# Kernel optimization log

Hardware: AMD Instinct MI355X
Metric: run time of the kernel (lower is better)

Reference implementation:

```python
import jax, jax.numpy as jnp
import numpy as np

B, NPG = 64, 512          # graphs, nodes per graph
N_TOTAL = B * NPG
LIG = 128                 # ligand nodes per graph (segment 0); rest are protein (segment 1)
BOX = 40.0                # Angstrom box for random coords -> realistic radius-graph density
INTER_CUTOFF = 10.0       # normalize_coord is identity (scale=1)
INTRA_CUTOFF = 8.0


def setup_inputs() -> dict:
    key = jax.random.key(0)
    X = jax.random.uniform(key, (N_TOTAL, 1, 3), dtype=jnp.float32) * BOX
    batch_id = jnp.repeat(jnp.arange(B, dtype=jnp.int32), NPG)
    local = jnp.tile(jnp.arange(NPG, dtype=jnp.int32), B)
    segment_id = (local >= LIG).astype(jnp.int32)
    is_global = jnp.logical_or(local == 0, local == LIG)  # one global node per segment
    return {"X": X, "batch_id": batch_id, "segment_id": segment_id, "is_global": is_global}


def _radial_edges(X, src_dst, cutoff):
    # src_dst: [E, 2] node indices; X: [N, C, 3], channel 0 holds coords
    p = X[:, 0][src_dst]                              # [E, 2, 3]
    dist = jnp.linalg.norm(p[:, 0] - p[:, 1], axis=-1)
    return src_dst[dist <= cutoff].T                  # [2, E']


def reference(X, batch_id, segment_id, is_global):
    N = batch_id.shape[0]
    nB = int(batch_id[-1]) + 1
    lengths = jax.ops.segment_sum(jnp.ones_like(batch_id), batch_id, num_segments=nB)
    max_n = int(jnp.max(lengths))
    offsets = jnp.concatenate([jnp.zeros((1,), lengths.dtype), jnp.cumsum(lengths)[:-1]])
    gni = jnp.arange(N)
    gni2lni = gni - offsets[batch_id]                 # local node index within its graph

    # Dense [N, max_n] same-batch mask via cumsum trick (O(N*max_n))
    same_bid = jnp.zeros((N, max_n), jnp.float32)
    same_bid = same_bid.at[gni, lengths[batch_id] - 1].set(1.0)
    same_bid = 1.0 - jnp.cumsum(same_bid, axis=-1)
    same_bid = jnp.concatenate([jnp.ones((N, 1), jnp.float32), same_bid[:, :-1]], axis=-1)
    same_bid = same_bid.at[gni, gni2lni].set(0.0)     # remove self edges

    row, col = jnp.nonzero(same_bid)                  # all same-graph candidate pairs
    col = col + offsets[batch_id[row]]                # local col -> global node index

    row_global = is_global[row]
    col_global = is_global[col]
    not_global = jnp.logical_not(jnp.logical_or(row_global, col_global))
    row_seg = segment_id[row]
    col_seg = segment_id[col]

    # intra-protein context edges (segment 1, within 8A)
    sel = (row_seg == col_seg) & (row_seg == 1) & not_global
    ctx_edges = _radial_edges(X, jnp.stack([row[sel], col[sel]], axis=1), INTRA_CUTOFF)

    # inter ligand-protein edges (within 10A)
    sel = (row_seg != col_seg) & not_global
    ir, ic = row[sel], col[sel]
    inter_edges = _radial_edges(X, jnp.stack([ir, ic], axis=1), INTER_CUTOFF)
    if inter_edges.shape[1] == 0:
        inter_edges = jnp.array([[ir[0], ic[0]], [ic[0], ir[0]]], dtype=inter_edges.dtype)

    reduced_inter_edge_batchid = batch_id[inter_edges[0][inter_edges[0] < inter_edges[1]]]
    reduced_inter_edge_offsets = offsets[reduced_inter_edge_batchid]

    # global<->same-segment edges and global<->global edges appended to context
    sel = (row_seg == col_seg) & jnp.logical_not(not_global)
    global_normal = jnp.stack([row[sel], col[sel]])
    sel = row_global & col_global
    global_global = jnp.stack([row[sel], col[sel]])
    ctx_edges = jnp.concatenate([ctx_edges, global_normal, global_global], axis=1)

    return ctx_edges, inter_edges, reduced_inter_edge_batchid, reduced_inter_edge_offsets
```

## Files before the change

### kernel.cpp

```cpp
#include <hip/hip_runtime.h>

#define NB 64
#define NPG 512
#define LIG 128
#define NBLK 1024
#define RPB 32
#define THREADS 512

__device__ __forceinline__ float dist2(float dx, float dy, float dz) {
    return __fadd_rn(__fadd_rn(__fmul_rn(dx, dx), __fmul_rn(dy, dy)), __fmul_rn(dz, dz));
}
#define T10 __uint_as_float(0x42C80001u)
#define T8  __uint_as_float(0x42800001u)

__global__ __launch_bounds__(THREADS) void count_kernel(const float* __restrict__ X,
                                                        unsigned long long* __restrict__ gmask,
                                                        int* __restrict__ bp) {
    __shared__ float s[NPG * 3];
    __shared__ unsigned long long smask[RPB * 8];
    __shared__ int rc[RPB], ri[RPB];
    const int b = blockIdx.x;
    const int g = b >> 4;
    const int h = b & 15;
    const int t = threadIdx.x;
    const int lane = t & 63;
    const int w = t >> 6;
    if (t < 384) ((float4*)s)[t] = ((const float4*)X)[g * 384 + t];
    if (t < RPB * 8) smask[t] = 0ull;
    __syncthreads();

    float cx[8], cy[8], cz[8];
#pragma unroll
    for (int k = 0; k < 8; ++k) {
        const int c = k * 64 + lane;
        cx[k] = s[3 * c]; cy[k] = s[3 * c + 1]; cz[k] = s[3 * c + 2];
    }

#pragma unroll
    for (int j = 0; j < 4; ++j) {
        const int lr = w * 4 + j;
        const int r = h * 32 + lr;
        const float px = s[3 * r], py = s[3 * r + 1], pz = s[3 * r + 2];
        int cc = 0, ci = 0;
        if (h < 4) {
            if (r != 0) {
                unsigned long long mm[6];
#pragma unroll
                for (int k = 2; k < 8; ++k) {
                    unsigned long long m =
                        __ballot(dist2(px - cx[k], py - cy[k], pz - cz[k]) <= T10);
                    if (k == 2) m &= ~1ull;
                    mm[k - 2] = m;
                    ci += __popcll(m);
                }
                if (lane == 0) {
#pragma unroll
                    for (int k = 0; k < 6; ++k) smask[lr * 8 + 2 + k] = mm[k];
                }
            }
        } else if (r != LIG) {
            unsigned long long mm[8];
#pragma unroll
            for (int k = 0; k < 2; ++k) {
                unsigned long long m =
                    __ballot(dist2(px - cx[k], py - cy[k], pz - cz[k]) <= T10);
                if (k == 0) m &= ~1ull;
                mm[k] = m;
                ci += __popcll(m);
            }
            const int kr = r >> 6;
            const unsigned long long selfbit = 1ull << (r & 63);
#pragma unroll
            for (int k = 2; k < 8; ++k) {
                unsigned long long m =
                    __ballot(dist2(px - cx[k], py - cy[k], pz - cz[k]) <= T8);
                if (k == 2) m &= ~1ull;
                if (k == kr) m &= ~selfbit;
                mm[k] = m;
                cc += __popcll(m);
            }
            if (lane == 0) {
#pragma unroll
                for (int k = 0; k < 8; ++k) smask[lr * 8 + k] = mm[k];
            }
        }
        if (lane == 0) { rc[lr] = cc; ri[lr] = ci; }
    }
    __syncthreads();
    if (t < RPB * 8) gmask[(size_t)b * (RPB * 8) + t] = smask[t];
    if (t < 64) {
        int c = (t < RPB) ? rc[t] : 0;
        int i = (t < RPB) ? ri[t] : 0;
#pragma unroll
        for (int off = 32; off >= 1; off >>= 1) {
            c += __shfl_down(c, off, 64);
            i += __shfl_down(i, off, 64);
        }
        if (t == 0) {
            bp[b] = c;
            bp[NBLK + b] = i;
            bp[2 * NBLK + b] = (h < 4) ? i : 0;
        }
    }
}

__global__ __launch_bounds__(THREADS) void emit_kernel(const unsigned long long* __restrict__ gmask,
                                                       const int* __restrict__ bp,
                                                       int* __restrict__ out) {
    __shared__ unsigned long long smask[RPB * 8];
    __shared__ int sc[RPB], si[RPB];
    __shared__ int blkb[3], tot[3], sint;
    const int b = blockIdx.x;
    const int g = b >> 4;
    const int h = b & 15;
    const int t = threadIdx.x;
    const int lane = t & 63;
    const int w = t >> 6;
    const unsigned long long lmask = (1ull << lane) - 1ull;
    const int gn = g * NPG;

    if (t < RPB * 8) smask[t] = gmask[(size_t)b * (RPB * 8) + t];

    if (w < 3) {
        const int base = w * NBLK + lane * 16;
        int v[16]; int sum = 0;
#pragma unroll
        for (int i = 0; i < 16; ++i) { v[i] = bp[base + i]; sum += v[i]; }
        int incl = sum;
#pragma unroll
        for (int off = 1; off < 64; off <<= 1) {
            int n = __shfl_up(incl, off, 64);
            if (lane >= off) incl += n;
        }
        if (lane == (b >> 4)) {
            int e = incl - sum;
            const int idx = b & 15;
            for (int i = 0; i < idx; ++i) e += v[i];
            blkb[w] = e;
        }
        if (lane == 63) tot[w] = incl;
    }
    __syncthreads();

    if (t < RPB) {
        int mc = 0, mi = 0;
        if (h < 4) {
#pragma unroll
            for (int k = 2; k < 8; ++k) mi += __popcll(smask[t * 8 + k]);
        } else {
            mi = __popcll(smask[t * 8 + 0]) + __popcll(smask[t * 8 + 1]);
#pragma unroll
            for (int k = 2; k < 8; ++k) mc += __popcll(smask[t * 8 + k]);
        }
        int ic = mc, ii = mi;
#pragma unroll
        for (int off = 1; off < 32; off <<= 1) {
            int a0 = __shfl_up(ic, off, 64);
            int a1 = __shfl_up(ii, off, 64);
            if (lane >= off) { ic += a0; ii += a1; }
        }
        sc[t] = blkb[0] + ic - mc;
        si[t] = blkb[1] + ii - mi;
        if (t == RPB - 1) sint = ii;
    }
    __syncthreads();

    const int Eci = tot[0];
    const int Ei  = tot[1];
    const int Er  = tot[2];
    const int Ectx = Eci + NB * 1020 + NB * 2;

    int* ctx_src   = out;
    int* ctx_dst   = out + Ectx;
    int* inter_src = out + 2 * Ectx;
    int* inter_dst = inter_src + Ei;
    int* red_bid   = out + 2 * Ectx + 2 * Ei;
    int* red_off   = red_bid + Er;

    for (int j = 0; j < 4; ++j) {
        const int lr = w * 4 + j;
        const int r = h * 32 + lr;
        const int row = gn + r;

        unsigned long long m[8];
#pragma unroll
        for (int k = 0; k < 8; ++k) m[k] = smask[lr * 8 + k];

        if (h < 4) {
            if (r == 0) {
                for (int k = 0; k < 2; ++k) {
                    const int c = k * 64 + lane;
                    if (c >= 1 && c < LIG) {
                        const int pos = Eci + g * 1020 + (c - 1);
                        ctx_src[pos] = row; ctx_dst[pos] = gn + c;
                    }
                }
                if (lane == 0) {
                    const int pos = Eci + NB * 1020 + g * 2;
                    ctx_src[pos] = row; ctx_dst[pos] = gn + LIG;
                }
            } else {
                int ib = si[lr];
#pragma unroll
                for (int k = 2; k < 8; ++k) {
                    if (m[k]) {
                        if ((m[k] >> lane) & 1ull) {
                            const int c = k * 64 + lane;
                            const int p = __popcll(m[k] & lmask);
                            inter_src[ib + p] = row; inter_dst[ib + p] = gn + c;
                        }
                        ib += __popcll(m[k]);
                    }
                }
                if (lane == 0) {
                    const int pos = Eci + g * 1020 + (LIG - 1) + (r - 1);
                    ctx_src[pos] = row; ctx_dst[pos] = gn;
                }
            }
        } else {
            if (r == LIG) {
                for (int k = 2; k < 8; ++k) {
                    const int c = k * 64 + lane;
                    if (c > LIG) {
                        const int pos = Eci + g * 1020 + 2 * (LIG - 1) + (c - LIG - 1);
                        ctx_src[pos] = row; ctx_dst[pos] = gn + c;
                    }
                }
                if (lane == 0) {
                    const int pos = Eci + NB * 1020 + g * 2 + 1;
                    ctx_src[pos] = row; ctx_dst[pos] = gn;
                }
            } else {
                int ib = si[lr];
#pragma unroll
                for (int k = 0; k < 2; ++k) {
                    if (m[k]) {
                        if ((m[k] >> lane) & 1ull) {
                            const int c = k * 64 + lane;
                            const int pos = ib + __popcll(m[k] & lmask);
                            inter_src[pos] = row; inter_dst[pos] = gn + c;
                        }
                        ib += __popcll(m[k]);
                    }
                }
                int cb = sc[lr];
#pragma unroll
                for (int k = 2; k < 8; ++k) {
                    if (m[k]) {
                        if ((m[k] >> lane) & 1ull) {
                            const int c = k * 64 + lane;
                            const int pos = cb + __popcll(m[k] & lmask);
                            ctx_src[pos] = row; ctx_dst[pos] = gn + c;
                        }
                        cb += __popcll(m[k]);
                    }
                }
                if (lane == 0) {
                    const int pos = Eci + g * 1020 + 2 * (LIG - 1) + (NPG - LIG - 1) + (r - LIG - 1);
                    ctx_src[pos] = row; ctx_dst[pos] = gn + LIG;
                }
            }
        }
    }

    if (h < 4) {
        const int rb0 = blkb[2];
        const int n = sint;
        for (int i = t; i < n; i += THREADS) {
            red_bid[rb0 + i] = g;
            red_off[rb0 + i] = gn;
        }
    }
}

extern "C" void kernel_launch(void* const* d_in, const int* in_sizes, int n_in,
                              void* d_out, int out_size, void* d_ws, size_t ws_size,
                              hipStream_t stream) {
    (void)in_sizes; (void)n_in; (void)out_size; (void)ws_size;
    const float* X = (const float*)d_in[0];
    int* ws = (int*)d_ws;
    int* bp = ws;
    unsigned long long* gmask =
        (unsigned long long*)(ws + 4096);
    int* out = (int*)d_out;

    count_kernel<<<NBLK, THREADS, 0, stream>>>(X, gmask, bp);
    emit_kernel<<<NBLK, THREADS, 0, stream>>>(gmask, bp, out);
}
```

Baseline: 79.84 us.

## Fuse count and emit kernels via in-kernel spin-waited global prefix scan

Merges the count and emit passes into one kernel. Each block publishes its packed (ctx, inter) counts with a flag bit to a workspace array, then spin-waits on all 1024 entries to compute its exclusive offsets, so the mask never round-trips through global memory and one launch is saved. Adds a memset launch, and correctness depends on all 1024 blocks being co-resident. That is attempted via launch_bounds(512,8), but a guard-limited spin could otherwise deadlock or produce wrong offsets. Counts are packed into 21-bit fields of a 64-bit word.

```diff
diff --git a/kernel.cpp b/kernel.cpp
--- a/kernel.cpp
+++ b/kernel.cpp
@@ -13,18 +13,32 @@
 #define T10 __uint_as_float(0x42C80001u)
 #define T8  __uint_as_float(0x42800001u)
 
-__global__ __launch_bounds__(THREADS) void count_kernel(const float* __restrict__ X,
-                                                        unsigned long long* __restrict__ gmask,
-                                                        int* __restrict__ bp) {
+#define F21 0x1FFFFFull
+
+__device__ __forceinline__ unsigned long long pk_triple(unsigned long long v, int j) {
+    unsigned long long ci = v & F21;
+    unsigned long long cc = (v >> 21) & F21;
+    unsigned long long red = (j < 4) ? ci : 0ull;
+    return (cc << 42) | (ci << 21) | red;
+}
+
+__global__ __launch_bounds__(THREADS, 8) void fused_kernel(const float* __restrict__ X,
+                                                           unsigned long long* __restrict__ pk,
+                                                           int* __restrict__ out) {
     __shared__ float s[NPG * 3];
     __shared__ unsigned long long smask[RPB * 8];
     __shared__ int rc[RPB], ri[RPB];
+    __shared__ int sc[RPB], si[RPB];
+    __shared__ unsigned long long sblkb, stot;
+    __shared__ int sint;
+
     const int b = blockIdx.x;
     const int g = b >> 4;
     const int h = b & 15;
     const int t = threadIdx.x;
     const int lane = t & 63;
     const int w = t >> 6;
+
     if (t < 384) ((float4*)s)[t] = ((const float4*)X)[g * 384 + t];
     if (t < RPB * 8) smask[t] = 0ull;
     __syncthreads();
@@ -87,71 +101,63 @@
         if (lane == 0) { rc[lr] = cc; ri[lr] = ci; }
     }
     __syncthreads();
-    if (t < RPB * 8) gmask[(size_t)b * (RPB * 8) + t] = smask[t];
-    if (t < 64) {
-        int c = (t < RPB) ? rc[t] : 0;
-        int i = (t < RPB) ? ri[t] : 0;
+
+    if (w == 0) {
+        int c = (lane < RPB) ? rc[lane] : 0;
+        int ii = (lane < RPB) ? ri[lane] : 0;
 #pragma unroll
         for (int off = 32; off >= 1; off >>= 1) {
             c += __shfl_down(c, off, 64);
-            i += __shfl_down(i, off, 64);
-        }
-        if (t == 0) {
-            bp[b] = c;
-            bp[NBLK + b] = i;
-            bp[2 * NBLK + b] = (h < 4) ? i : 0;
-        }
-    }
-}
-
-__global__ __launch_bounds__(THREADS) void emit_kernel(const unsigned long long* __restrict__ gmask,
-                                                       const int* __restrict__ bp,
-                                                       int* __restrict__ out) {
-    __shared__ unsigned long long smask[RPB * 8];
-    __shared__ int sc[RPB], si[RPB];
-    __shared__ int blkb[3], tot[3], sint;
-    const int b = blockIdx.x;
-    const int g = b >> 4;
-    const int h = b & 15;
-    const int t = threadIdx.x;
-    const int lane = t & 63;
-    const int w = t >> 6;
-    const unsigned long long lmask = (1ull << lane) - 1ull;
-    const int gn = g * NPG;
-
-    if (t < RPB * 8) smask[t] = gmask[(size_t)b * (RPB * 8) + t];
-
-    if (w < 3) {
-        const int base = w * NBLK + lane * 16;
-        int v[16]; int sum = 0;
-#pragma unroll
-        for (int i = 0; i < 16; ++i) { v[i] = bp[base + i]; sum += v[i]; }
-        int incl = sum;
+            ii += __shfl_down(ii, off, 64);
+        }
+        if (lane == 0) {
+            const unsigned long long q = (1ull << 63) |
+                ((unsigned long long)(unsigned)c << 21) | (unsigned long long)(unsigned)ii;
+            __hip_atomic_store(&pk[b], q, __ATOMIC_RELAXED, __HIP_MEMORY_SCOPE_AGENT);
+        }
+        const int base = lane * 16;
+        unsigned long long sum = 0;
+#pragma unroll
+        for (int j = 0; j < 16; ++j) {
+            unsigned long long v =
+                __hip_atomic_load(&pk[base + j], __ATOMIC_RELAXED, __HIP_MEMORY_SCOPE_AGENT);
+            int guard = 0;
+            while (!(v >> 63) && ++guard < (1 << 20)) {
+                __builtin_amdgcn_s_sleep(8);
+                v = __hip_atomic_load(&pk[base + j], __ATOMIC_RELAXED, __HIP_MEMORY_SCOPE_AGENT);
+            }
+            sum += pk_triple(v, j);
+        }
+        unsigned long long incl = sum;
 #pragma unroll
         for (int off = 1; off < 64; off <<= 1) {
-            int n = __shfl_up(incl, off, 64);
+            unsigned long long n = __shfl_up(incl, off, 64);
             if (lane >= off) incl += n;
         }
         if (lane == (b >> 4)) {
-            int e = incl - sum;
+            unsigned long long e = incl - sum;
             const int idx = b & 15;
-            for (int i = 0; i < idx; ++i) e += v[i];
-            blkb[w] = e;
-        }
-        if (lane == 63) tot[w] = incl;
-    }
-    __syncthreads();
+            for (int jj = 0; jj < idx; ++jj) {
+                unsigned long long v =
+                    __hip_atomic_load(&pk[base + jj], __ATOMIC_RELAXED, __HIP_MEMORY_SCOPE_AGENT);
+                e += pk_triple(v, jj);
+            }
+            sblkb = e;
+        }
+        if (lane == 63) stot = incl;
+    }
+    __syncthreads();
+
+    const int blkb0 = (int)((sblkb >> 42) & F21);
+    const int blkb1 = (int)((sblkb >> 21) & F21);
+    const int blkb2 = (int)(sblkb & F21);
+    const int Eci = (int)((stot >> 42) & F21);
+    const int Ei  = (int)((stot >> 21) & F21);
+    const int Er  = (int)(stot & F21);
 
     if (t < RPB) {
-        int mc = 0, mi = 0;
-        if (h < 4) {
-#pragma unroll
-            for (int k = 2; k < 8; ++k) mi += __popcll(smask[t * 8 + k]);
-        } else {
-            mi = __popcll(smask[t * 8 + 0]) + __popcll(smask[t * 8 + 1]);
-#pragma unroll
-            for (int k = 2; k < 8; ++k) mc += __popcll(smask[t * 8 + k]);
-        }
+        const int mc = rc[t];
+        const int mi = ri[t];
         int ic = mc, ii = mi;
 #pragma unroll
         for (int off = 1; off < 32; off <<= 1) {
@@ -159,15 +165,14 @@
             int a1 = __shfl_up(ii, off, 64);
             if (lane >= off) { ic += a0; ii += a1; }
         }
-        sc[t] = blkb[0] + ic - mc;
-        si[t] = blkb[1] + ii - mi;
+        sc[t] = blkb0 + ic - mc;
+        si[t] = blkb1 + ii - mi;
         if (t == RPB - 1) sint = ii;
     }
     __syncthreads();
 
-    const int Eci = tot[0];
-    const int Ei  = tot[1];
-    const int Er  = tot[2];
+    const unsigned long long lmask = (1ull << lane) - 1ull;
+    const int gn = g * NPG;
     const int Ectx = Eci + NB * 1020 + NB * 2;
 
     int* ctx_src   = out;
@@ -264,7 +269,7 @@
     }
 
     if (h < 4) {
-        const int rb0 = blkb[2];
+        const int rb0 = blkb2;
         const int n = sint;
         for (int i = t; i < n; i += THREADS) {
             red_bid[rb0 + i] = g;
@@ -278,12 +283,9 @@
                               hipStream_t stream) {
     (void)in_sizes; (void)n_in; (void)out_size; (void)ws_size;
     const float* X = (const float*)d_in[0];
-    int* ws = (int*)d_ws;
-    int* bp = ws;
-    unsigned long long* gmask =
-        (unsigned long long*)(ws + 4096);
+    unsigned long long* pk = (unsigned long long*)d_ws;
     int* out = (int*)d_out;
 
-    count_kernel<<<NBLK, THREADS, 0, stream>>>(X, gmask, bp);
-    emit_kernel<<<NBLK, THREADS, 0, stream>>>(gmask, bp, out);
-}
+    hipMemsetAsync(pk, 0, NBLK * sizeof(unsigned long long), stream);
+    fused_kernel<<<NBLK, THREADS, 0, stream>>>(X, pk, out);
+}
```

Result: slower. 85.84 us (+7.5%).
